# Performance work log

Measured on AMD Instinct MI355X. Metric: run time of the kernel, lower is better.

The kernel has to match this reference:

```python
import jax, jax.numpy as jnp
import numpy as np

N_NODES = 50000
N_EDGES = 1600000
IN_DIM = 64
EDGE_DIM = 8
N_GRAPHS = 256
EXP_IN = 32
H = 64  # hidden dim per head / GCN hidden
EPS = 1e-5
NEG_SLOPE = 0.2


def gat_layer(x, src, dst, ea, W, a_src, a_dst, We, a_e, bias, heads, dim, concat):
    """PyG-style GATConv with edge features and self-loops (fill_value='mean')."""
    N = x.shape[0]
    ones_e = jnp.ones((ea.shape[0],), x.dtype)
    cnt = jax.ops.segment_sum(ones_e, dst, num_segments=N)
    loop_attr = jax.ops.segment_sum(ea, dst, num_segments=N) / jnp.maximum(cnt, 1.0)[:, None]
    s = jnp.concatenate([src, jnp.arange(N)])
    d = jnp.concatenate([dst, jnp.arange(N)])
    eaf = jnp.concatenate([ea, loop_attr], axis=0)  # [E+N, edge_dim]
    h = (x @ W).reshape(N, heads, dim)              # [N, H, D]
    ee = (eaf @ We).reshape(-1, heads, dim)         # [E+N, H, D]
    al_src = (h * a_src).sum(-1)                    # [N, H]
    al_dst = (h * a_dst).sum(-1)                    # [N, H]
    score = al_src[s] + al_dst[d] + (ee * a_e).sum(-1)
    score = jax.nn.leaky_relu(score, NEG_SLOPE)     # [E+N, H]
    m = jax.ops.segment_max(score, d, num_segments=N)
    ex = jnp.exp(score - m[d])
    att = ex / jax.ops.segment_sum(ex, d, num_segments=N)[d]
    out = jax.ops.segment_sum(h[s] * att[:, :, None], d, num_segments=N)  # [N, H, D]
    out = out.reshape(N, heads * dim) if concat else out.mean(axis=1)
    return out + bias


def gcn_layer(x, src, dst, W, b):
    """PyG-style GCNConv: add self loops, symmetric degree normalization."""
    N = x.shape[0]
    s = jnp.concatenate([src, jnp.arange(N)])
    d = jnp.concatenate([dst, jnp.arange(N)])
    deg = jax.ops.segment_sum(jnp.ones((s.shape[0],), x.dtype), d, num_segments=N)
    dinv = jax.lax.rsqrt(deg)  # deg >= 1 thanks to self loops
    norm = dinv[s] * dinv[d]
    h = x @ W
    return jax.ops.segment_sum(h[s] * norm[:, None], d, num_segments=N) + b


def bn(x, g, b):
    m = x.mean(axis=0)
    v = x.var(axis=0)
    return g * (x - m) * jax.lax.rsqrt(v + EPS) + b


def mean_pool(x, batch, num_graphs):
    s = jax.ops.segment_sum(x, batch, num_segments=num_graphs)
    c = jax.ops.segment_sum(jnp.ones((x.shape[0],), x.dtype), batch, num_segments=num_graphs)
    return s / jnp.maximum(c, 1.0)[:, None]


def setup_inputs() -> dict:
    key = jax.random.key(0)
    ks = jax.random.split(key, 32)
    p = lambda i, shape: jax.random.normal(ks[i], shape, jnp.float32) * 0.05
    z = lambda n: jnp.zeros((n,), jnp.float32)
    o = lambda n: jnp.ones((n,), jnp.float32)
    return {
        "x": jax.random.normal(ks[0], (N_NODES, IN_DIM), jnp.float32),
        "edge_attr": jax.random.normal(ks[1], (N_EDGES, EDGE_DIM), jnp.float32),
        "experimental_feat": jax.random.normal(ks[2], (N_GRAPHS, EXP_IN), jnp.float32),
        "edge_index": jax.random.randint(ks[3], (2, N_EDGES), 0, N_NODES),
        "batch": jnp.sort(jax.random.randint(ks[4], (N_NODES,), 0, N_GRAPHS)),
        "W1": p(5, (IN_DIM, 4 * H)), "att_src1": p(6, (4, H)), "att_dst1": p(7, (4, H)),
        "We1": p(8, (EDGE_DIM, 4 * H)), "att_e1": p(9, (4, H)), "b1": z(4 * H),
        "g1": o(4 * H), "be1": z(4 * H),
        "W2": p(10, (4 * H, H)), "att_src2": p(11, (1, H)), "att_dst2": p(12, (1, H)),
        "We2": p(13, (EDGE_DIM, H)), "att_e2": p(14, (1, H)), "b2": z(H),
        "g2": o(H), "be2": z(H),
        "Wg1": p(15, (H, H)), "bg1": z(H), "g3": o(H), "be3": z(H),
        "Wg2": p(16, (H, H)), "bg2": z(H), "g4": o(H), "be4": z(H),
        "Wex1": p(17, (EXP_IN, H)), "bex1": z(H), "Wex2": p(18, (H, H)), "bex2": z(H),
        "Wc1": p(19, (2 * H, 128)), "bc1": z(128), "Wc2": p(20, (128, 1)), "bc2": z(1),
    }


def reference(x, edge_attr, experimental_feat, edge_index, batch,
              W1, att_src1, att_dst1, We1, att_e1, b1, g1, be1,
              W2, att_src2, att_dst2, We2, att_e2, b2, g2, be2,
              Wg1, bg1, g3, be3, Wg2, bg2, g4, be4,
              Wex1, bex1, Wex2, bex2, Wc1, bc1, Wc2, bc2):
    src, dst = edge_index[0], edge_index[1]
    h = gat_layer(x, src, dst, edge_attr, W1, att_src1, att_dst1, We1, att_e1, b1, 4, H, True)
    h = jax.nn.relu(bn(h, g1, be1))
    h = gat_layer(h, src, dst, edge_attr, W2, att_src2, att_dst2, We2, att_e2, b2, 1, H, False)
    h = jax.nn.relu(bn(h, g2, be2))  # dropout = identity in eval
    h = gcn_layer(h, src, dst, Wg1, bg1)
    h = jax.nn.relu(bn(h, g3, be3))
    h = gcn_layer(h, src, dst, Wg2, bg2)
    h = jax.nn.relu(bn(h, g4, be4))
    xp = mean_pool(h, batch, N_GRAPHS)                    # [G, H]
    e = jax.nn.relu(experimental_feat @ Wex1 + bex1)
    e = jax.nn.relu(e @ Wex2 + bex2)
    combined = jnp.concatenate([xp, e], axis=1)           # [G, 2H]
    combined = jax.nn.relu(combined @ Wc1 + bc1)          # [G, 128]
    out = combined @ Wc2 + bc2                            # [G, 1]
    return (out, xp, combined)
```

## Files before the change

### kernel.cpp

```cpp
#include <hip/hip_runtime.h>
#include <hip/hip_bf16.h>

#define N_NODES 50000
#define N_EDGES 1600000
#define N_GRAPHS 256
#define NEG_SLOPE 0.2f
#define BN_EPS 1e-5f

typedef __hip_bfloat16 bf16;
typedef __attribute__((ext_vector_type(8))) short s16x8;
typedef __attribute__((ext_vector_type(4))) float f32x4;
typedef __attribute__((ext_vector_type(4))) int i32x4;
typedef __attribute__((ext_vector_type(4))) unsigned u32x4;

__device__ __forceinline__ float b2f(bf16 v){ return __bfloat162float(v); }
__device__ __forceinline__ bf16 f2b(float v){ return __float2bfloat16(v); }
__device__ __forceinline__ float us2f(unsigned short u){ return __uint_as_float(((unsigned)u)<<16); }
__device__ __forceinline__ unsigned short f2us(float v){ bf16 b = f2b(v); return *(unsigned short*)&b; }
__device__ __forceinline__ unsigned pk2(float a, float b){ return (unsigned)f2us(a) | ((unsigned)f2us(b)<<16); }
__device__ __forceinline__ float ldF(const void* p, size_t i, int m){
  return m ? ((const float*)p)[i] : b2f(((const bf16*)p)[i]);
}
__device__ __forceinline__ float sane(float v){
  return (v == v && fabsf(v) < 1e30f) ? v : 0.f;
}
__device__ __forceinline__ float sel4(const float v[4], int h){
  float r = v[0];
  r = (h==1) ? v[1] : r;
  r = (h==2) ? v[2] : r;
  r = (h==3) ? v[3] : r;
  return r;
}
__device__ __forceinline__ void acc8(float* acc, float w, uint4 u){
  acc[0] += w*us2f((unsigned short)(u.x & 0xffff)); acc[1] += w*us2f((unsigned short)(u.x >> 16));
  acc[2] += w*us2f((unsigned short)(u.y & 0xffff)); acc[3] += w*us2f((unsigned short)(u.y >> 16));
  acc[4] += w*us2f((unsigned short)(u.z & 0xffff)); acc[5] += w*us2f((unsigned short)(u.z >> 16));
  acc[6] += w*us2f((unsigned short)(u.w & 0xffff)); acc[7] += w*us2f((unsigned short)(u.w >> 16));
}
__device__ __forceinline__ void unp8(float* o, uint4 u){
  o[0] = us2f((unsigned short)(u.x & 0xffff)); o[1] = us2f((unsigned short)(u.x >> 16));
  o[2] = us2f((unsigned short)(u.y & 0xffff)); o[3] = us2f((unsigned short)(u.y >> 16));
  o[4] = us2f((unsigned short)(u.z & 0xffff)); o[5] = us2f((unsigned short)(u.z >> 16));
  o[6] = us2f((unsigned short)(u.w & 0xffff)); o[7] = us2f((unsigned short)(u.w >> 16));
}
__device__ __forceinline__ s16x8 pk8(const float* v){
  s16x8 r;
  #pragma unroll
  for(int j=0;j<8;j++) r[j] = (short)f2us(v[j]);
  return r;
}

__device__ int detect_mode_block(const void* x){
  __shared__ int s_ins;
  if(threadIdx.x == 0) s_ins = 0;
  __syncthreads();
  const unsigned short* u = (const unsigned short*)x;
  int c = 0;
  for(int i = threadIdx.x; i < 1024; i += blockDim.x){
    float v = fabsf(us2f(u[i]));
    if(!(v > 1e-6f && v < 1e4f)) c++;
  }
  if(c) atomicAdd(&s_ins, c);
  __syncthreads();
  return (s_ins > 128) ? 1 : 0;
}

#define NSEG 33
struct Bank { const void* p[NSEG]; int n[NSEG]; int off[NSEG]; };

__global__ void k_convert(Bank b, const void* xdet, float* out){
  int m = detect_mode_block(xdet);
  int seg = blockIdx.y;
  int i = blockIdx.x*256 + threadIdx.x;
  if(i < b.n[seg]) out[b.off[seg] + i] = ldF(b.p[seg], i, m);
}

__global__ void k_cvt_x(const void* x, bf16* xb){
  int m = detect_mode_block(x);
  int i4 = blockIdx.x*256 + threadIdx.x;
  if(i4 >= N_NODES*16) return;
  if(m){
    float4 v = ((const float4*)x)[i4];
    ((ushort4*)xb)[i4] = make_ushort4(f2us(v.x), f2us(v.y), f2us(v.z), f2us(v.w));
  } else {
    ((ushort4*)xb)[i4] = ((const ushort4*)x)[i4];
  }
}

__global__ void k_we(const float* __restrict__ We1, const float* __restrict__ ae1,
                     const float* __restrict__ We2, const float* __restrict__ ae2,
                     float* __restrict__ w_e){
  int t = threadIdx.x;
  if(t < 32){
    int h = t >> 3, k = t & 7;
    float s = 0.f;
    for(int d=0;d<64;d++) s += We1[k*256 + h*64 + d] * ae1[h*64 + d];
    w_e[t] = s;
  } else if(t < 40){
    int k = t - 32;
    float s = 0.f;
    for(int d=0;d<64;d++) s += We2[k*64 + d] * ae2[d];
    w_e[t] = s;
  }
}

__global__ void k_wt(const float* __restrict__ W1, const float* __restrict__ W2,
                     const float* __restrict__ Wg1, const float* __restrict__ Wg2,
                     bf16* __restrict__ wt){
  int i = blockIdx.x*256 + threadIdx.x;
  if(i < 16384){
    int c = i >> 6, k = i & 63;
    wt[i] = f2b(W1[k*256 + c]);
  } else if(i < 32768){
    int j = i - 16384; int c = j >> 8, k = j & 255;
    wt[i] = f2b(W2[k*64 + c]);
  } else if(i < 36864){
    int j = i - 32768; int c = j >> 6, k = j & 63;
    wt[i] = f2b(Wg1[k*64 + c]);
  } else if(i < 40960){
    int j = i - 36864; int c = j >> 6, k = j & 63;
    wt[i] = f2b(Wg2[k*64 + c]);
  }
}

__global__ void k_count(const int* __restrict__ dst, int* __restrict__ cnt){
  int e = blockIdx.x*256 + threadIdx.x;
  if(e < N_EDGES){
    int d = dst[e]; if((unsigned)d >= N_NODES) d = 0;
    atomicAdd(&cnt[d], 1);
  }
}

__global__ void k_blocksum(const int* __restrict__ cnt, int* __restrict__ bsum){
  __shared__ int s[256];
  int i = blockIdx.x*256 + threadIdx.x;
  s[threadIdx.x] = (i < N_NODES) ? cnt[i] : 0;
  __syncthreads();
  for(int o=128;o>0;o>>=1){ if(threadIdx.x<o) s[threadIdx.x]+=s[threadIdx.x+o]; __syncthreads(); }
  if(threadIdx.x==0) bsum[blockIdx.x]=s[0];
}

__global__ void k_scan_bsum(const int* __restrict__ bsum, int* __restrict__ bofs, int nb){
  __shared__ int s[256];
  int t = threadIdx.x;
  s[t] = (t<nb) ? bsum[t] : 0;
  __syncthreads();
  for(int o=1;o<256;o<<=1){ int v=(t>=o)?s[t-o]:0; __syncthreads(); s[t]+=v; __syncthreads(); }
  bofs[t] = (t==0) ? 0 : s[t-1];
}

__global__ void k_scan_write(const int* __restrict__ cnt, const int* __restrict__ bofs,
                             int* __restrict__ rp, float* __restrict__ dinv){
  __shared__ int s[256];
  int t = threadIdx.x; int i = blockIdx.x*256 + t;
  int v = (i<N_NODES) ? cnt[i] : 0;
  s[t]=v; __syncthreads();
  for(int o=1;o<256;o<<=1){ int a=(t>=o)?s[t-o]:0; __syncthreads(); s[t]+=a; __syncthreads(); }
  if(i<N_NODES){
    rp[i+1] = s[t] + bofs[blockIdx.x];
    dinv[i] = rsqrtf((float)v + 1.f);
  }
  if(i==0) rp[0]=0;
}

__global__ void k_fill(const int* __restrict__ src, const int* __restrict__ dst,
                       const int* __restrict__ rp, int* __restrict__ fill,
                       const void* __restrict__ ea, const void* __restrict__ xdet,
                       const float* __restrict__ w_e,
                       int4* __restrict__ epk){
  int m = detect_mode_block(xdet);
  int e = blockIdx.x*256 + threadIdx.x;
  if(e >= N_EDGES) return;
  int d = dst[e]; if((unsigned)d >= N_NODES) d = 0;
  int p = atomicAdd(&fill[d], 1);
  int slot = rp[d] + p;
  if((unsigned)slot >= N_EDGES) return;
  int sv = src[e]; if((unsigned)sv >= N_NODES) sv = 0;
  float a[8];
  if(m){
    const float* eaf = (const float*)ea;
    float4 lo = *(const float4*)&eaf[(size_t)e*8];
    float4 hi = *(const float4*)&eaf[(size_t)e*8 + 4];
    a[0]=lo.x; a[1]=lo.y; a[2]=lo.z; a[3]=lo.w;
    a[4]=hi.x; a[5]=hi.y; a[6]=hi.z; a[7]=hi.w;
  } else {
    #pragma unroll
    for(int k=0;k<8;k++) a[k] = b2f(((const bf16*)ea)[(size_t)e*8 + k]);
  }
  unsigned d4[4];
  #pragma unroll
  for(int h=0;h<4;h++){
    float s = 0.f;
    #pragma unroll
    for(int k=0;k<8;k++) s += a[k]*w_e[h*8+k];
    d4[h] = f2us(s);
  }
  float s1 = 0.f;
  #pragma unroll
  for(int k=0;k<8;k++) s1 += a[k]*w_e[32+k];
  i32x4 pk;
  pk[0] = sv;
  pk[1] = (int)(d4[0] | (d4[1] << 16));
  pk[2] = (int)(d4[2] | (d4[3] << 16));
  pk[3] = (int)(unsigned)f2us(s1);
  __builtin_nontemporal_store(pk, (i32x4*)&epk[slot]);
}

__global__ __launch_bounds__(256) void k_gemmA_mfma(
    const bf16* __restrict__ xb,
    const bf16* __restrict__ wt1,
    bf16* __restrict__ hp, int M)
{
  const int tid = threadIdx.x;
  const int w = tid >> 6, l = tid & 63;
  const int lr = l & 15, lg = l >> 4;
  const int bm = blockIdx.x*64 + w*16;
  const int arow_i = bm + lr;
  const uint4* arow = (const uint4*)(xb + (size_t)min(arow_i, M-1)*64);
  uint4 a0u = arow[lg];
  uint4 a1u = arow[4 + lg];
  s16x8 a0 = *(s16x8*)&a0u, a1 = *(s16x8*)&a1u;
  unsigned short* out = (unsigned short*)hp;
  const int orow0 = bm + lg*4;
  #pragma unroll
  for(int ct = 0; ct < 16; ct++){
    const uint4* brow = (const uint4*)(wt1 + (size_t)(ct*16 + lr)*64);
    uint4 b0u = brow[lg];
    uint4 b1u = brow[4 + lg];
    f32x4 acc = {0.f, 0.f, 0.f, 0.f};
    acc = __builtin_amdgcn_mfma_f32_16x16x32_bf16(a0, *(s16x8*)&b0u, acc, 0, 0, 0);
    acc = __builtin_amdgcn_mfma_f32_16x16x32_bf16(a1, *(s16x8*)&b1u, acc, 0, 0, 0);
    #pragma unroll
    for(int r = 0; r < 4; r++){
      int rr = orow0 + r;
      if(rr < M) out[(size_t)rr*256 + ct*16 + lr] = f2us(acc[r]);
    }
  }
}

template<int KIN>
__global__ __launch_bounds__(256) void k_gemmB_mfma(
    const bf16* __restrict__ A, const bf16* __restrict__ Wt,
    bf16* __restrict__ C, int M,
    const float* __restrict__ bnsums, const float* __restrict__ bng, const float* __restrict__ bnb)
{
  __shared__ float st_s[KIN];
  __shared__ float st_t[KIN];
  const int tid = threadIdx.x;
  if(tid < KIN){
    const float invN = 1.0f / (float)N_NODES;
    float mean = bnsums[tid]*invN;
    float var  = fmaxf(bnsums[KIN+tid]*invN - mean*mean, 0.f);
    float s = bng[tid]*rsqrtf(var + BN_EPS);
    st_s[tid] = s;
    st_t[tid] = bnb[tid] - mean*s;
  }
  __syncthreads();
  const int w = tid >> 6, l = tid & 63;
  const int lr = l & 15, lg = l >> 4;
  const int bm = blockIdx.x*64 + w*16;
  const int arow_i = bm + lr;
  const uint4* arow = (const uint4*)(A + (size_t)min(arow_i, M-1)*KIN);
  f32x4 acc[4];
  #pragma unroll
  for(int ct=0;ct<4;ct++) acc[ct] = (f32x4){0.f,0.f,0.f,0.f};
  #pragma unroll
  for(int k0 = 0; k0 < KIN; k0 += 32){
    uint4 au = arow[(k0 >> 3) + lg];
    int c0 = k0 + lg*8;
    float v[8]; unp8(v, au);
    #pragma unroll
    for(int j = 0; j < 8; j++){
      float y = sane(v[j])*st_s[c0+j] + st_t[c0+j];
      v[j] = fmaxf(y, 0.f);
    }
    s16x8 af = pk8(v);
    #pragma unroll
    for(int ct = 0; ct < 4; ct++){
      const uint4* brow = (const uint4*)(Wt + (size_t)(ct*16 + lr)*KIN);
      uint4 bu = brow[(k0 >> 3) + lg];
      acc[ct] = __builtin_amdgcn_mfma_f32_16x16x32_bf16(af, *(s16x8*)&bu, acc[ct], 0, 0, 0);
    }
  }
  unsigned short* out = (unsigned short*)C;
  const int orow0 = bm + lg*4;
  #pragma unroll
  for(int ct = 0; ct < 4; ct++){
    #pragma unroll
    for(int r = 0; r < 4; r++){
      int rr = orow0 + r;
      if(rr < M) out[(size_t)rr*64 + ct*16 + lr] = f2us(acc[ct][r]);
    }
  }
}

__global__ void k_al4(const bf16* __restrict__ hp, const float* __restrict__ asrc,
                      const float* __restrict__ adst,
                      float* __restrict__ als4, float* __restrict__ ald4){
  int idx = blockIdx.x*256 + threadIdx.x;
  if(idx >= N_NODES*4) return;
  int n = idx >> 2, h = idx & 3;
  const unsigned short* row = (const unsigned short*)hp + (size_t)n*256 + h*64;
  float ss=0.f, sd=0.f;
  #pragma unroll
  for(int q=0;q<16;q++){
    ushort4 u = *(const ushort4*)&row[4*q];
    float4 a_s = *(const float4*)&asrc[h*64 + 4*q];
    float4 a_d = *(const float4*)&adst[h*64 + 4*q];
    float v0=us2f(u.x), v1=us2f(u.y), v2=us2f(u.z), v3=us2f(u.w);
    ss += v0*a_s.x + v1*a_s.y + v2*a_s.z + v3*a_s.w;
    sd += v0*a_d.x + v1*a_d.y + v2*a_d.z + v3*a_d.w;
  }
  als4[idx]=ss; ald4[idx]=sd;
}

__global__ void k_al1(const bf16* __restrict__ hp, const float* __restrict__ asrc,
                      const float* __restrict__ adst,
                      float* __restrict__ als, float* __restrict__ ald){
  int n = blockIdx.x*256 + threadIdx.x;
  if(n >= N_NODES) return;
  const unsigned short* row = (const unsigned short*)hp + (size_t)n*64;
  float ss=0.f, sd=0.f;
  #pragma unroll
  for(int q=0;q<16;q++){
    ushort4 u = *(const ushort4*)&row[4*q];
    float4 a_s = *(const float4*)&asrc[4*q];
    float4 a_d = *(const float4*)&adst[4*q];
    float v0=us2f(u.x), v1=us2f(u.y), v2=us2f(u.z), v3=us2f(u.w);
    ss += v0*a_s.x + v1*a_s.y + v2*a_s.z + v3*a_s.w;
    sd += v0*a_d.x + v1*a_d.y + v2*a_d.z + v3*a_d.w;
  }
  als[n]=ss; ald[n]=sd;
}

__global__ __launch_bounds__(64) void k_gat_agg4(
    const int* __restrict__ rp, const int4* __restrict__ epk,
    const bf16* __restrict__ hp,
    const float* __restrict__ als4, const float* __restrict__ ald4,
    const float* __restrict__ bias256, bf16* __restrict__ out1){
  int n = blockIdx.x; int t = threadIdx.x;
  int eh = t >> 5, c8 = t & 31;
  int head = c8 >> 3;
  __shared__ int   ssrc[64];
  __shared__ float swt[64][4];
  int s0 = rp[n], e0 = rp[n+1];
  if((unsigned)s0 > N_EDGES){ s0=0; e0=0; }
  if(e0 < s0 || (unsigned)e0 > N_EDGES) e0 = s0;
  float4 aldv = *(const float4*)&ald4[n*4];
  float4 alsvn = *(const float4*)&als4[n*4];
  float wsum[4] = {0.f,0.f,0.f,0.f};
  float dsum[4] = {0.f,0.f,0.f,0.f};
  float acc[8]  = {0.f,0.f,0.f,0.f,0.f,0.f,0.f,0.f};
  const unsigned short* hpu = (const unsigned short*)hp;

  for(int base = s0; base < e0; base += 64){
    int m = min(64, e0 - base);
    if(t < m){
      i32x4 pk = __builtin_nontemporal_load((const i32x4*)&epk[base+t]);
      int sn = pk[0]; if((unsigned)sn >= N_NODES) sn = 0;
      ssrc[t] = sn;
      float edf[4] = {us2f((unsigned short)(pk[1] & 0xffff)), us2f((unsigned short)((unsigned)pk[1] >> 16)),
                      us2f((unsigned short)(pk[2] & 0xffff)), us2f((unsigned short)((unsigned)pk[2] >> 16))};
      float4 alss = *(const float4*)&als4[sn*4];
      float alssv[4] = {alss.x, alss.y, alss.z, alss.w};
      float aldvv[4] = {aldv.x, aldv.y, aldv.z, aldv.w};
      float w4[4];
      #pragma unroll
      for(int h=0;h<4;h++){
        float sc = alssv[h] + aldvv[h] + edf[h];
        sc = sc > 0.f ? sc : NEG_SLOPE*sc;
        sc = fminf(sc, 30.f);
        float w = __expf(sc);
        w4[h] = w;
        wsum[h] += w; dsum[h] += edf[h];
      }
      *(float4*)&swt[t][0] = make_float4(w4[0], w4[1], w4[2], w4[3]);
    }
    __syncthreads();
    #pragma unroll 8
    for(int i=0;i<m;i+=2){
      int j = i + eh;
      if(j < m){
        int row = ssrc[j];
        float w = swt[j][head];
        uint4 u = *(const uint4*)&hpu[(size_t)row*256 + 8*c8];
        acc8(acc, w, u);
      }
    }
    __syncthreads();
  }
  #pragma unroll
  for(int o=1;o<64;o<<=1){
    #pragma unroll
    for(int h=0;h<4;h++){
      wsum[h] += __shfl_xor(wsum[h], o);
      dsum[h] += __shfl_xor(dsum[h], o);
    }
  }
  #pragma unroll
  for(int q=0;q<8;q++) acc[q] += __shfl_xor(acc[q], 32);
  if(eh == 0){
    float alsnv[4] = {alsvn.x, alsvn.y, alsvn.z, alsvn.w};
    float aldnv[4] = {aldv.x, aldv.y, aldv.z, aldv.w};
    float sEh = sel4(wsum, head), sDh = sel4(dsum, head);
    float deg = (float)(e0 - s0);
    float sdot = deg > 0.f ? sDh/deg : 0.f;
    float sc = sel4(alsnv, head) + sel4(aldnv, head) + sdot;
    sc = sc > 0.f ? sc : NEG_SLOPE*sc;
    sc = fminf(sc, 30.f);
    float wself = __expf(sc);
    float self[8];
    unp8(self, *(const uint4*)&hpu[(size_t)n*256 + 8*c8]);
    float4 b0 = *(const float4*)&bias256[8*c8];
    float4 b1 = *(const float4*)&bias256[8*c8 + 4];
    float bi[8] = {b0.x,b0.y,b0.z,b0.w,b1.x,b1.y,b1.z,b1.w};
    float inv = 1.f/(sEh + wself);
    float o8[8];
    #pragma unroll
    for(int q=0;q<8;q++) o8[q] = (acc[q] + wself*self[q])*inv + bi[q];
    u32x4 st;
    st[0] = pk2(o8[0],o8[1]); st[1] = pk2(o8[2],o8[3]);
    st[2] = pk2(o8[4],o8[5]); st[3] = pk2(o8[6],o8[7]);
    __builtin_nontemporal_store(st, (u32x4*)&((unsigned short*)out1)[(size_t)n*256 + 8*c8]);
  }
}

__global__ __launch_bounds__(64) void k_gat_agg1e(
    const int* __restrict__ rp, const int4* __restrict__ epk,
    const bf16* __restrict__ hp,
    const float* __restrict__ als, const float* __restrict__ ald,
    const float* __restrict__ bias64, bf16* __restrict__ out){
  int n = blockIdx.x; int t = threadIdx.x;
  int eg = t >> 3, c8 = t & 7;
  __shared__ float sw[64];
  __shared__ int   ssrc[64];
  int s0 = rp[n], e0 = rp[n+1];
  if((unsigned)s0 > N_EDGES){ s0=0; e0=0; }
  if(e0 < s0 || (unsigned)e0 > N_EDGES) e0 = s0;
  float aldn = ald[n];
  float wsum_l = 0.f, dsum_l = 0.f;
  float acc[8] = {0.f,0.f,0.f,0.f,0.f,0.f,0.f,0.f};
  const unsigned short* hpu = (const unsigned short*)hp;
  for(int base = s0; base < e0; base += 64){
    int m = min(64, e0 - base);
    if(t < m){
      i32x4 pk = __builtin_nontemporal_load((const i32x4*)&epk[base+t]);
      int sn = pk[0]; if((unsigned)sn >= N_NODES) sn = 0;
      ssrc[t] = sn;
      float ed = us2f((unsigned short)(pk[3] & 0xffff));
      float sc = als[sn] + aldn + ed;
      sc = sc > 0.f ? sc : NEG_SLOPE*sc;
      sc = fminf(sc, 30.f);
      float w = __expf(sc);
      sw[t] = w;
      wsum_l += w; dsum_l += ed;
    }
    __syncthreads();
    #pragma unroll 4
    for(int i=0;i<m;i+=8){
      int j = i + eg;
      if(j < m){
        int row = ssrc[j];
        float w = sw[j];
        uint4 u = *(const uint4*)&hpu[(size_t)row*64 + 8*c8];
        acc8(acc, w, u);
      }
    }
    __syncthreads();
  }
  #pragma unroll
  for(int o=1;o<64;o<<=1){ wsum_l += __shfl_xor(wsum_l, o); dsum_l += __shfl_xor(dsum_l, o); }
  #pragma unroll
  for(int q=0;q<8;q++){
    acc[q] += __shfl_xor(acc[q], 8);
    acc[q] += __shfl_xor(acc[q], 16);
    acc[q] += __shfl_xor(acc[q], 32);
  }
  if(t < 8){
    float deg = (float)(e0 - s0);
    float sdot = deg > 0.f ? dsum_l/deg : 0.f;
    float sc = als[n] + aldn + sdot;
    sc = sc > 0.f ? sc : NEG_SLOPE*sc;
    sc = fminf(sc, 30.f);
    float wself = __expf(sc);
    float self[8];
    unp8(self, *(const uint4*)&hpu[(size_t)n*64 + 8*t]);
    float4 b0 = *(const float4*)&bias64[8*t];
    float4 b1 = *(const float4*)&bias64[8*t + 4];
    float bi[8] = {b0.x,b0.y,b0.z,b0.w,b1.x,b1.y,b1.z,b1.w};
    float inv = 1.f/(wsum_l + wself);
    float o8[8];
    #pragma unroll
    for(int q=0;q<8;q++) o8[q] = (acc[q] + wself*self[q])*inv + bi[q];
    u32x4 st;
    st[0] = pk2(o8[0],o8[1]); st[1] = pk2(o8[2],o8[3]);
    st[2] = pk2(o8[4],o8[5]); st[3] = pk2(o8[6],o8[7]);
    __builtin_nontemporal_store(st, (u32x4*)&((unsigned short*)out)[(size_t)n*64 + 8*t]);
  }
}

__global__ __launch_bounds__(64) void k_gcn_agg(
    const int* __restrict__ rp, const int4* __restrict__ epk,
    const float* __restrict__ dinv, const bf16* __restrict__ gp,
    const float* __restrict__ bias, bf16* __restrict__ out){
  int n = blockIdx.x; int t = threadIdx.x;
  int eg = t >> 3, c8 = t & 7;
  __shared__ float sw[64];
  __shared__ int   ssrc[64];
  int s0 = rp[n], e0 = rp[n+1];
  if((unsigned)s0 > N_EDGES){ s0=0; e0=0; }
  if(e0 < s0 || (unsigned)e0 > N_EDGES) e0 = s0;
  float dn = dinv[n];
  float acc[8] = {0.f,0.f,0.f,0.f,0.f,0.f,0.f,0.f};
  const unsigned short* gpu = (const unsigned short*)gp;
  for(int base = s0; base < e0; base += 64){
    int m = min(64, e0 - base);
    if(t < m){
      i32x4 pk = __builtin_nontemporal_load((const i32x4*)&epk[base+t]);
      int sn = pk[0]; if((unsigned)sn >= N_NODES) sn = 0;
      ssrc[t]=sn; sw[t]=dinv[sn];
    }
    __syncthreads();
    #pragma unroll 4
    for(int i=0;i<m;i+=8){
      int j = i + eg;
      if(j < m){
        int row = ssrc[j];
        float w = sw[j];
        uint4 u = *(const uint4*)&gpu[(size_t)row*64 + 8*c8];
        acc8(acc, w, u);
      }
    }
    __syncthreads();
  }
  #pragma unroll
  for(int q=0;q<8;q++){
    acc[q] += __shfl_xor(acc[q], 8);
    acc[q] += __shfl_xor(acc[q], 16);
    acc[q] += __shfl_xor(acc[q], 32);
  }
  if(t < 8){
    float self[8];
    unp8(self, *(const uint4*)&gpu[(size_t)n*64 + 8*t]);
    float4 b0 = *(const float4*)&bias[8*t];
    float4 b1 = *(const float4*)&bias[8*t + 4];
    float bi[8] = {b0.x,b0.y,b0.z,b0.w,b1.x,b1.y,b1.z,b1.w};
    float o8[8];
    #pragma unroll
    for(int q=0;q<8;q++) o8[q] = dn*(acc[q] + dn*self[q]) + bi[q];
    u32x4 st;
    st[0] = pk2(o8[0],o8[1]); st[1] = pk2(o8[2],o8[3]);
    st[2] = pk2(o8[4],o8[5]); st[3] = pk2(o8[6],o8[7]);
    __builtin_nontemporal_store(st, (u32x4*)&((unsigned short*)out)[(size_t)n*64 + 8*t]);
  }
}

template<int C>
__global__ void k_colstats(const bf16* __restrict__ X, float* __restrict__ sums){
  constexpr int RPB = 128;
  constexpr int RSTEP = 256 / C;
  int c = threadIdx.x % C;
  int r0 = threadIdx.x / C;
  int rbeg = blockIdx.x * RPB;
  int rend = min(N_NODES, rbeg + RPB);
  const unsigned short* Xu = (const unsigned short*)X;
  float s = 0.f, q = 0.f;
  for(int r = rbeg + r0; r < rend; r += RSTEP){
    float v = sane(us2f(Xu[(size_t)r*C + c]));
    s += v; q += v*v;
  }
  atomicAdd(&sums[c], s);
  atomicAdd(&sums[C + c], q);
}

__global__ __launch_bounds__(64) void k_pool3(
    const bf16* __restrict__ h, const int* __restrict__ batch,
    const float* __restrict__ sums, const float* __restrict__ g4,
    const float* __restrict__ b4,
    float* __restrict__ psum, float* __restrict__ pcnt){
  int t = threadIdx.x;
  int n0 = blockIdx.x * 256;
  int n1 = min(N_NODES, n0 + 256);
  if(n0 >= n1) return;
  const float invN = 1.0f / (float)N_NODES;
  float mean = sums[t]*invN;
  float var = fmaxf(sums[64+t]*invN - mean*mean, 0.f);
  float rstd = rsqrtf(var + BN_EPS);
  float gg = g4[t], bb = b4[t];
  const unsigned short* hu = (const unsigned short*)h;
  int cur = batch[n0]; if((unsigned)cur >= N_GRAPHS) cur = 0;
  float acc = 0.f; int cl = 0;
  for(int n = n0; n < n1; n++){
    int g = batch[n]; if((unsigned)g >= N_GRAPHS) g = 0;
    if(g != cur){
      atomicAdd(&psum[cur*64 + t], acc);
      if(t == 0) atomicAdd(&pcnt[cur], (float)cl);
      acc = 0.f; cl = 0; cur = g;
    }
    float y = (sane(us2f(hu[(size_t)n*64 + t]))-mean)*rstd*gg + bb;
    acc += fmaxf(y, 0.f);
    cl++;
  }
  atomicAdd(&psum[cur*64 + t], acc);
  if(t == 0) atomicAdd(&pcnt[cur], (float)cl);
}

__device__ __forceinline__ void stO(void* o, size_t i, float v, int m){
  if(m) ((float*)o)[i] = v; else ((bf16*)o)[i] = f2b(v);
}

__global__ __launch_bounds__(128) void k_head(
    const float* __restrict__ psum, const float* __restrict__ pcnt,
    const float* __restrict__ exf,
    const float* __restrict__ Wex1, const float* __restrict__ bex1,
    const float* __restrict__ Wex2, const float* __restrict__ bex2,
    const float* __restrict__ Wc1, const float* __restrict__ bc1,
    const float* __restrict__ Wc2, const float* __restrict__ bc2,
    const void* __restrict__ xdet, void* __restrict__ dout){
  int m0 = detect_mode_block(xdet);
  int g = blockIdx.x; int t = threadIdx.x;
  __shared__ float ci[128];
  __shared__ float e1[64];
  __shared__ float comb[128];
  __shared__ float red[128];
  if(t < 64){
    float c = fmaxf(pcnt[g], 1.f);
    float xp = sane(psum[g*64 + t]) / c;
    ci[t] = xp;
    stO(dout, 256 + (size_t)g*64 + t, xp, m0);
  } else {
    int j = t - 64;
    float s = bex1[j];
    for(int k=0;k<32;k++) s += exf[g*32 + k] * Wex1[k*64 + j];
    e1[j] = fmaxf(s, 0.f);
  }
  __syncthreads();
  if(t >= 64){
    int j = t - 64;
    float s = bex2[j];
    for(int k=0;k<64;k++) s += e1[k] * Wex2[k*64 + j];
    ci[64 + j] = fmaxf(s, 0.f);
  }
  __syncthreads();
  {
    float s = bc1[t];
    for(int k=0;k<128;k++) s += ci[k] * Wc1[k*128 + t];
    s = fmaxf(s, 0.f);
    comb[t] = s;
    stO(dout, 256 + 16384 + (size_t)g*128 + t, s, m0);
  }
  __syncthreads();
  red[t] = comb[t] * Wc2[t];
  __syncthreads();
  for(int o=64;o>0;o>>=1){ if(t<o) red[t]+=red[t+o]; __syncthreads(); }
  if(t==0) stO(dout, g, red[0] + bc2[0], m0);
}

extern "C" void kernel_launch(void* const* d_in, const int* in_sizes, int n_in,
                              void* d_out, int out_size, void* d_ws, size_t ws_size,
                              hipStream_t stream){
  const void* x    = d_in[0];
  const void* ea   = d_in[1];
  const int* ei    = (const int*)d_in[3];
  const int* batch = (const int*)d_in[4];
  const int* src = ei;
  const int* dst = ei + N_EDGES;

  char* base = (char*)d_ws;
  size_t off = 0;
  auto alloc = [&](size_t bytes) -> void* {
    void* r = base + off;
    off += (bytes + 255) & ~(size_t)255;
    return r;
  };
  int*   cnt    = (int*)  alloc((size_t)N_NODES*4);
  int*   fill   = (int*)  alloc((size_t)N_NODES*4);
  float* bnstat = (float*)alloc(4096);
  float* pool   = (float*)alloc((size_t)(N_GRAPHS*64 + N_GRAPHS)*4);
  size_t zbytes = off;
  int*   rp      = (int*)  alloc((size_t)(N_NODES+1)*4);
  int*   bsum    = (int*)  alloc(256*4);
  int*   bofs    = (int*)  alloc(256*4);
  int4*  epk     = (int4*) alloc((size_t)N_EDGES*16);
  float* dinv    = (float*)alloc((size_t)N_NODES*4);
  float* w_e     = (float*)alloc(64*4);
  float* als4    = (float*)alloc((size_t)N_NODES*4*4);
  float* ald4    = (float*)alloc((size_t)N_NODES*4*4);
  float* wbank   = (float*)alloc(80000*4);
  bf16*  wt      = (bf16*) alloc((size_t)40960*2);
  bf16*  xb      = (bf16*) alloc((size_t)N_NODES*64*2);
  bf16*  hp      = (bf16*) alloc((size_t)N_NODES*256*2);
  bf16*  outb    = (bf16*) alloc((size_t)N_NODES*256*2);

  bf16* out1 = outb;
  bf16* out2 = outb;
  bf16* out3 = outb + (size_t)N_NODES*64;
  bf16* out4 = outb + (size_t)N_NODES*128;
  float* bn1 = bnstat;
  float* bn2 = bnstat + 512;
  float* bn3 = bnstat + 640;
  float* bn4 = bnstat + 768;
  float* psum = pool;
  float* pcnt = pool + N_GRAPHS*64;

  bf16* wt1  = wt;
  bf16* wt2  = wt + 16384;
  bf16* wtg1 = wt + 32768;
  bf16* wtg2 = wt + 36864;

  const int segidx[NSEG] = {2, 5,6,7,8,9,10,11,12, 13,14,15,16,17,18,19,20,
                            21,22,23,24, 25,26,27,28, 29,30,31,32, 33,34,35,36};
  const int segn[NSEG] = {8192, 16384,256,256,2048,256,256,256,256,
                          16384,64,64,512,64,64,64,64,
                          4096,64,64,64, 4096,64,64,64,
                          2048,64,4096,64, 16384,128,128,1};
  Bank bk;
  int offs[NSEG]; int acc0 = 0;
  for(int i=0;i<NSEG;i++){ bk.p[i]=d_in[segidx[i]]; bk.n[i]=segn[i]; bk.off[i]=acc0; offs[i]=acc0; acc0+=segn[i]; }
  const float* f_exf = wbank + offs[0];
  const float* fW1 = wbank+offs[1]; const float* fas1 = wbank+offs[2]; const float* fad1 = wbank+offs[3];
  const float* fWe1= wbank+offs[4]; const float* fae1 = wbank+offs[5]; const float* fb1  = wbank+offs[6];
  const float* fg1 = wbank+offs[7]; const float* fbe1 = wbank+offs[8];
  const float* fW2 = wbank+offs[9]; const float* fas2 = wbank+offs[10]; const float* fad2 = wbank+offs[11];
  const float* fWe2= wbank+offs[12]; const float* fae2 = wbank+offs[13]; const float* fb2 = wbank+offs[14];
  const float* fg2 = wbank+offs[15]; const float* fbe2 = wbank+offs[16];
  const float* fWg1= wbank+offs[17]; const float* fbg1 = wbank+offs[18]; const float* fg3 = wbank+offs[19];
  const float* fbe3= wbank+offs[20];
  const float* fWg2= wbank+offs[21]; const float* fbg2 = wbank+offs[22]; const float* fg4 = wbank+offs[23];
  const float* fbe4= wbank+offs[24];
  const float* fWex1=wbank+offs[25]; const float* fbex1= wbank+offs[26];
  const float* fWex2=wbank+offs[27]; const float* fbex2= wbank+offs[28];
  const float* fWc1= wbank+offs[29]; const float* fbc1 = wbank+offs[30];
  const float* fWc2= wbank+offs[31]; const float* fbc2 = wbank+offs[32];

  const int nbN  = (N_NODES + 255)/256;
  const int nbE  = (N_EDGES + 255)/256;
  const int nbT  = (N_NODES + 63)/64;

  hipMemsetAsync(d_ws, 0, zbytes, stream);
  {
    dim3 g((16384+255)/256, NSEG);
    k_convert<<<g,256,0,stream>>>(bk, x, wbank);
  }
  k_wt<<<160,256,0,stream>>>(fW1, fW2, fWg1, fWg2, wt);
  k_cvt_x<<<(N_NODES*16+255)/256,256,0,stream>>>(x, xb);
  k_we<<<1,64,0,stream>>>(fWe1, fae1, fWe2, fae2, w_e);
  k_count<<<nbE,256,0,stream>>>(dst, cnt);
  k_blocksum<<<nbN,256,0,stream>>>(cnt, bsum);
  k_scan_bsum<<<1,256,0,stream>>>(bsum, bofs, nbN);
  k_scan_write<<<nbN,256,0,stream>>>(cnt, bofs, rp, dinv);
  k_fill<<<nbE,256,0,stream>>>(src, dst, rp, fill, ea, x, w_e, epk);

  k_gemmA_mfma<<<nbT,256,0,stream>>>(xb, wt1, hp, N_NODES);
  k_al4<<<(N_NODES*4+255)/256,256,0,stream>>>(hp, fas1, fad1, als4, ald4);
  k_gat_agg4<<<N_NODES,64,0,stream>>>(rp, epk, hp, als4, ald4, fb1, out1);
  k_colstats<256><<<(N_NODES+127)/128,256,0,stream>>>(out1, bn1);

  k_gemmB_mfma<256><<<nbT,256,0,stream>>>(out1, wt2, hp, N_NODES, bn1, fg1, fbe1);
  k_al1<<<nbN,256,0,stream>>>(hp, fas2, fad2, als4, ald4);
  k_gat_agg1e<<<N_NODES,64,0,stream>>>(rp, epk, hp, als4, ald4, fb2, out2);
  k_colstats<64><<<(N_NODES+127)/128,256,0,stream>>>(out2, bn2);

  k_gemmB_mfma<64><<<nbT,256,0,stream>>>(out2, wtg1, hp, N_NODES, bn2, fg2, fbe2);
  k_gcn_agg<<<N_NODES,64,0,stream>>>(rp, epk, dinv, hp, fbg1, out3);
  k_colstats<64><<<(N_NODES+127)/128,256,0,stream>>>(out3, bn3);

  k_gemmB_mfma<64><<<nbT,256,0,stream>>>(out3, wtg2, hp, N_NODES, bn3, fg3, fbe3);
  k_gcn_agg<<<N_NODES,64,0,stream>>>(rp, epk, dinv, hp, fbg2, out4);
  k_colstats<64><<<(N_NODES+127)/128,256,0,stream>>>(out4, bn4);

  k_pool3<<<nbN,64,0,stream>>>(out4, batch, bn4, fg4, fbe4, psum, pcnt);
  k_head<<<N_GRAPHS,128,0,stream>>>(psum, pcnt, f_exf, fWex1, fbex1, fWex2, fbex2,
                                    fWc1, fbc1, fWc2, fbc2, x, (void*)d_out);
}
```

Baseline: 978.0 us.

## Fuse attention logits into GEMMs and pack four nodes per aggregation block

The per-node attention dot products (als/ald) are now computed inside the MFMA GEMM epilogues from fp32 accumulators, using cross-lane shuffles, which removes the separate k_al4/k_al1 kernels and their re-read of hp. The GAT and GCN aggregation kernels change from one 64-thread block per node to 256-thread blocks holding four independent waves, one node per wave. Block-wide __syncthreads are replaced with wave-local LDS fences. Nontemporal output stores become plain stores. The logits now use unrounded fp32 values instead of the bf16-rounded hp, and the wave-level fences rely on each wave working only on its own LDS slice.

```diff
diff --git a/kernel.cpp b/kernel.cpp
--- a/kernel.cpp
+++ b/kernel.cpp
@@ -11,7 +11,6 @@
 typedef __attribute__((ext_vector_type(8))) short s16x8;
 typedef __attribute__((ext_vector_type(4))) float f32x4;
 typedef __attribute__((ext_vector_type(4))) int i32x4;
-typedef __attribute__((ext_vector_type(4))) unsigned u32x4;
 
 __device__ __forceinline__ float b2f(bf16 v){ return __bfloat162float(v); }
 __device__ __forceinline__ bf16 f2b(float v){ return __float2bfloat16(v); }
@@ -48,6 +47,11 @@
   #pragma unroll
   for(int j=0;j<8;j++) r[j] = (short)f2us(v[j]);
   return r;
+}
+__device__ __forceinline__ void wave_lds_fence(){
+  __builtin_amdgcn_sched_barrier(0);
+  asm volatile("s_waitcnt lgkmcnt(0)" ::: "memory");
+  __builtin_amdgcn_sched_barrier(0);
 }
 
 __device__ int detect_mode_block(const void* x){
@@ -209,7 +213,10 @@
 __global__ __launch_bounds__(256) void k_gemmA_mfma(
     const bf16* __restrict__ xb,
     const bf16* __restrict__ wt1,
-    bf16* __restrict__ hp, int M)
+    bf16* __restrict__ hp, int M,
+    const float* __restrict__ asrc,
+    const float* __restrict__ adst,
+    float* __restrict__ als4, float* __restrict__ ald4)
 {
   const int tid = threadIdx.x;
   const int w = tid >> 6, l = tid & 63;
@@ -222,6 +229,8 @@
   s16x8 a0 = *(s16x8*)&a0u, a1 = *(s16x8*)&a1u;
   unsigned short* out = (unsigned short*)hp;
   const int orow0 = bm + lg*4;
+  float p_s[4][4] = {};
+  float p_d[4][4] = {};
   #pragma unroll
   for(int ct = 0; ct < 16; ct++){
     const uint4* brow = (const uint4*)(wt1 + (size_t)(ct*16 + lr)*64);
@@ -230,10 +239,38 @@
     f32x4 acc = {0.f, 0.f, 0.f, 0.f};
     acc = __builtin_amdgcn_mfma_f32_16x16x32_bf16(a0, *(s16x8*)&b0u, acc, 0, 0, 0);
     acc = __builtin_amdgcn_mfma_f32_16x16x32_bf16(a1, *(s16x8*)&b1u, acc, 0, 0, 0);
+    float a_s = asrc[ct*16 + lr];
+    float a_d = adst[ct*16 + lr];
+    int hh = ct >> 2;
     #pragma unroll
     for(int r = 0; r < 4; r++){
+      p_s[hh][r] += acc[r]*a_s;
+      p_d[hh][r] += acc[r]*a_d;
       int rr = orow0 + r;
       if(rr < M) out[(size_t)rr*256 + ct*16 + lr] = f2us(acc[r]);
+    }
+  }
+  #pragma unroll
+  for(int o = 1; o < 16; o <<= 1){
+    #pragma unroll
+    for(int hh=0; hh<4; hh++)
+      #pragma unroll
+      for(int r=0; r<4; r++){
+        p_s[hh][r] += __shfl_xor(p_s[hh][r], o);
+        p_d[hh][r] += __shfl_xor(p_d[hh][r], o);
+      }
+  }
+  if(lr == 0){
+    #pragma unroll
+    for(int r=0;r<4;r++){
+      int rr = orow0 + r;
+      if(rr < M){
+        #pragma unroll
+        for(int hh=0;hh<4;hh++){
+          als4[rr*4 + hh] = p_s[hh][r];
+          ald4[rr*4 + hh] = p_d[hh][r];
+        }
+      }
     }
   }
 }
@@ -242,7 +279,9 @@
 __global__ __launch_bounds__(256) void k_gemmB_mfma(
     const bf16* __restrict__ A, const bf16* __restrict__ Wt,
     bf16* __restrict__ C, int M,
-    const float* __restrict__ bnsums, const float* __restrict__ bng, const float* __restrict__ bnb)
+    const float* __restrict__ bnsums, const float* __restrict__ bng, const float* __restrict__ bnb,
+    const float* __restrict__ asrc, const float* __restrict__ adst,
+    float* __restrict__ als, float* __restrict__ ald)
 {
   __shared__ float st_s[KIN];
   __shared__ float st_t[KIN];
@@ -292,57 +331,51 @@
       if(rr < M) out[(size_t)rr*64 + ct*16 + lr] = f2us(acc[ct][r]);
     }
   }
-}
-
-__global__ void k_al4(const bf16* __restrict__ hp, const float* __restrict__ asrc,
-                      const float* __restrict__ adst,
-                      float* __restrict__ als4, float* __restrict__ ald4){
-  int idx = blockIdx.x*256 + threadIdx.x;
-  if(idx >= N_NODES*4) return;
-  int n = idx >> 2, h = idx & 3;
-  const unsigned short* row = (const unsigned short*)hp + (size_t)n*256 + h*64;
-  float ss=0.f, sd=0.f;
-  #pragma unroll
-  for(int q=0;q<16;q++){
-    ushort4 u = *(const ushort4*)&row[4*q];
-    float4 a_s = *(const float4*)&asrc[h*64 + 4*q];
-    float4 a_d = *(const float4*)&adst[h*64 + 4*q];
-    float v0=us2f(u.x), v1=us2f(u.y), v2=us2f(u.z), v3=us2f(u.w);
-    ss += v0*a_s.x + v1*a_s.y + v2*a_s.z + v3*a_s.w;
-    sd += v0*a_d.x + v1*a_d.y + v2*a_d.z + v3*a_d.w;
-  }
-  als4[idx]=ss; ald4[idx]=sd;
-}
-
-__global__ void k_al1(const bf16* __restrict__ hp, const float* __restrict__ asrc,
-                      const float* __restrict__ adst,
-                      float* __restrict__ als, float* __restrict__ ald){
-  int n = blockIdx.x*256 + threadIdx.x;
-  if(n >= N_NODES) return;
-  const unsigned short* row = (const unsigned short*)hp + (size_t)n*64;
-  float ss=0.f, sd=0.f;
-  #pragma unroll
-  for(int q=0;q<16;q++){
-    ushort4 u = *(const ushort4*)&row[4*q];
-    float4 a_s = *(const float4*)&asrc[4*q];
-    float4 a_d = *(const float4*)&adst[4*q];
-    float v0=us2f(u.x), v1=us2f(u.y), v2=us2f(u.z), v3=us2f(u.w);
-    ss += v0*a_s.x + v1*a_s.y + v2*a_s.z + v3*a_s.w;
-    sd += v0*a_d.x + v1*a_d.y + v2*a_d.z + v3*a_d.w;
-  }
-  als[n]=ss; ald[n]=sd;
-}
-
-__global__ __launch_bounds__(64) void k_gat_agg4(
+  if(als){
+    float p_s[4] = {0.f,0.f,0.f,0.f};
+    float p_d[4] = {0.f,0.f,0.f,0.f};
+    #pragma unroll
+    for(int ct=0;ct<4;ct++){
+      float a_s = asrc[ct*16 + lr];
+      float a_d = adst[ct*16 + lr];
+      #pragma unroll
+      for(int r=0;r<4;r++){
+        p_s[r] += acc[ct][r]*a_s;
+        p_d[r] += acc[ct][r]*a_d;
+      }
+    }
+    #pragma unroll
+    for(int o = 1; o < 16; o <<= 1){
+      #pragma unroll
+      for(int r=0;r<4;r++){
+        p_s[r] += __shfl_xor(p_s[r], o);
+        p_d[r] += __shfl_xor(p_d[r], o);
+      }
+    }
+    if(lr == 0){
+      #pragma unroll
+      for(int r=0;r<4;r++){
+        int rr = orow0 + r;
+        if(rr < M){ als[rr] = p_s[r]; ald[rr] = p_d[r]; }
+      }
+    }
+  }
+}
+
+__global__ __launch_bounds__(256) void k_gat_agg4(
     const int* __restrict__ rp, const int4* __restrict__ epk,
     const bf16* __restrict__ hp,
     const float* __restrict__ als4, const float* __restrict__ ald4,
     const float* __restrict__ bias256, bf16* __restrict__ out1){
-  int n = blockIdx.x; int t = threadIdx.x;
-  int eh = t >> 5, c8 = t & 31;
+  const int wid = threadIdx.x >> 6, l = threadIdx.x & 63;
+  const int n = blockIdx.x*4 + wid;
+  if(n >= N_NODES) return;
+  int eh = l >> 5, c8 = l & 31;
   int head = c8 >> 3;
-  __shared__ int   ssrc[64];
-  __shared__ float swt[64][4];
+  __shared__ int   ssrc_s[4][64];
+  __shared__ float swt_s[4][64][4];
+  int* ssrc = ssrc_s[wid];
+  float (*swt)[4] = swt_s[wid];
   int s0 = rp[n], e0 = rp[n+1];
   if((unsigned)s0 > N_EDGES){ s0=0; e0=0; }
   if(e0 < s0 || (unsigned)e0 > N_EDGES) e0 = s0;
@@ -355,10 +388,10 @@
 
   for(int base = s0; base < e0; base += 64){
     int m = min(64, e0 - base);
-    if(t < m){
-      i32x4 pk = __builtin_nontemporal_load((const i32x4*)&epk[base+t]);
+    if(l < m){
+      i32x4 pk = __builtin_nontemporal_load((const i32x4*)&epk[base+l]);
       int sn = pk[0]; if((unsigned)sn >= N_NODES) sn = 0;
-      ssrc[t] = sn;
+      ssrc[l] = sn;
       float edf[4] = {us2f((unsigned short)(pk[1] & 0xffff)), us2f((unsigned short)((unsigned)pk[1] >> 16)),
                       us2f((unsigned short)(pk[2] & 0xffff)), us2f((unsigned short)((unsigned)pk[2] >> 16))};
       float4 alss = *(const float4*)&als4[sn*4];
@@ -374,9 +407,9 @@
         w4[h] = w;
         wsum[h] += w; dsum[h] += edf[h];
       }
-      *(float4*)&swt[t][0] = make_float4(w4[0], w4[1], w4[2], w4[3]);
-    }
-    __syncthreads();
+      *(float4*)&swt[l][0] = make_float4(w4[0], w4[1], w4[2], w4[3]);
+    }
+    wave_lds_fence();
     #pragma unroll 8
     for(int i=0;i<m;i+=2){
       int j = i + eh;
@@ -387,7 +420,7 @@
         acc8(acc, w, u);
       }
     }
-    __syncthreads();
+    __builtin_amdgcn_wave_barrier();
   }
   #pragma unroll
   for(int o=1;o<64;o<<=1){
@@ -418,22 +451,26 @@
     float o8[8];
     #pragma unroll
     for(int q=0;q<8;q++) o8[q] = (acc[q] + wself*self[q])*inv + bi[q];
-    u32x4 st;
-    st[0] = pk2(o8[0],o8[1]); st[1] = pk2(o8[2],o8[3]);
-    st[2] = pk2(o8[4],o8[5]); st[3] = pk2(o8[6],o8[7]);
-    __builtin_nontemporal_store(st, (u32x4*)&((unsigned short*)out1)[(size_t)n*256 + 8*c8]);
-  }
-}
-
-__global__ __launch_bounds__(64) void k_gat_agg1e(
+    uint4 st;
+    st.x = pk2(o8[0],o8[1]); st.y = pk2(o8[2],o8[3]);
+    st.z = pk2(o8[4],o8[5]); st.w = pk2(o8[6],o8[7]);
+    *(uint4*)&((unsigned short*)out1)[(size_t)n*256 + 8*c8] = st;
+  }
+}
+
+__global__ __launch_bounds__(256) void k_gat_agg1e(
     const int* __restrict__ rp, const int4* __restrict__ epk,
     const bf16* __restrict__ hp,
     const float* __restrict__ als, const float* __restrict__ ald,
     const float* __restrict__ bias64, bf16* __restrict__ out){
-  int n = blockIdx.x; int t = threadIdx.x;
-  int eg = t >> 3, c8 = t & 7;
-  __shared__ float sw[64];
-  __shared__ int   ssrc[64];
+  const int wid = threadIdx.x >> 6, l = threadIdx.x & 63;
+  const int n = blockIdx.x*4 + wid;
+  if(n >= N_NODES) return;
+  int eg = l >> 3, c8 = l & 7;
+  __shared__ float sw_s[4][64];
+  __shared__ int   ssrc_s[4][64];
+  float* sw = sw_s[wid];
+  int* ssrc = ssrc_s[wid];
   int s0 = rp[n], e0 = rp[n+1];
   if((unsigned)s0 > N_EDGES){ s0=0; e0=0; }
   if(e0 < s0 || (unsigned)e0 > N_EDGES) e0 = s0;
@@ -443,19 +480,19 @@
   const unsigned short* hpu = (const unsigned short*)hp;
   for(int base = s0; base < e0; base += 64){
     int m = min(64, e0 - base);
-    if(t < m){
-      i32x4 pk = __builtin_nontemporal_load((const i32x4*)&epk[base+t]);
+    if(l < m){
+      i32x4 pk = __builtin_nontemporal_load((const i32x4*)&epk[base+l]);
       int sn = pk[0]; if((unsigned)sn >= N_NODES) sn = 0;
-      ssrc[t] = sn;
+      ssrc[l] = sn;
       float ed = us2f((unsigned short)(pk[3] & 0xffff));
       float sc = als[sn] + aldn + ed;
       sc = sc > 0.f ? sc : NEG_SLOPE*sc;
       sc = fminf(sc, 30.f);
       float w = __expf(sc);
-      sw[t] = w;
+      sw[l] = w;
       wsum_l += w; dsum_l += ed;
     }
-    __syncthreads();
+    wave_lds_fence();
     #pragma unroll 4
     for(int i=0;i<m;i+=8){
       int j = i + eg;
@@ -466,7 +503,7 @@
         acc8(acc, w, u);
       }
     }
-    __syncthreads();
+    __builtin_amdgcn_wave_barrier();
   }
   #pragma unroll
   for(int o=1;o<64;o<<=1){ wsum_l += __shfl_xor(wsum_l, o); dsum_l += __shfl_xor(dsum_l, o); }
@@ -476,7 +513,7 @@
     acc[q] += __shfl_xor(acc[q], 16);
     acc[q] += __shfl_xor(acc[q], 32);
   }
-  if(t < 8){
+  if(l < 8){
     float deg = (float)(e0 - s0);
     float sdot = deg > 0.f ? dsum_l/deg : 0.f;
     float sc = als[n] + aldn + sdot;
@@ -484,29 +521,33 @@
     sc = fminf(sc, 30.f);
     float wself = __expf(sc);
     float self[8];
-    unp8(self, *(const uint4*)&hpu[(size_t)n*64 + 8*t]);
-    float4 b0 = *(const float4*)&bias64[8*t];
-    float4 b1 = *(const float4*)&bias64[8*t + 4];
+    unp8(self, *(const uint4*)&hpu[(size_t)n*64 + 8*l]);
+    float4 b0 = *(const float4*)&bias64[8*l];
+    float4 b1 = *(const float4*)&bias64[8*l + 4];
     float bi[8] = {b0.x,b0.y,b0.z,b0.w,b1.x,b1.y,b1.z,b1.w};
     float inv = 1.f/(wsum_l + wself);
     float o8[8];
     #pragma unroll
     for(int q=0;q<8;q++) o8[q] = (acc[q] + wself*self[q])*inv + bi[q];
-    u32x4 st;
-    st[0] = pk2(o8[0],o8[1]); st[1] = pk2(o8[2],o8[3]);
-    st[2] = pk2(o8[4],o8[5]); st[3] = pk2(o8[6],o8[7]);
-    __builtin_nontemporal_store(st, (u32x4*)&((unsigned short*)out)[(size_t)n*64 + 8*t]);
-  }
-}
-
-__global__ __launch_bounds__(64) void k_gcn_agg(
+    uint4 st;
+    st.x = pk2(o8[0],o8[1]); st.y = pk2(o8[2],o8[3]);
+    st.z = pk2(o8[4],o8[5]); st.w = pk2(o8[6],o8[7]);
+    *(uint4*)&((unsigned short*)out)[(size_t)n*64 + 8*l] = st;
+  }
+}
+
+__global__ __launch_bounds__(256) void k_gcn_agg(
     const int* __restrict__ rp, const int4* __restrict__ epk,
     const float* __restrict__ dinv, const bf16* __restrict__ gp,
     const float* __restrict__ bias, bf16* __restrict__ out){
-  int n = blockIdx.x; int t = threadIdx.x;
-  int eg = t >> 3, c8 = t & 7;
-  __shared__ float sw[64];
-  __shared__ int   ssrc[64];
+  const int wid = threadIdx.x >> 6, l = threadIdx.x & 63;
+  const int n = blockIdx.x*4 + wid;
+  if(n >= N_NODES) return;
+  int eg = l >> 3, c8 = l & 7;
+  __shared__ float sw_s[4][64];
+  __shared__ int   ssrc_s[4][64];
+  float* sw = sw_s[wid];
+  int* ssrc = ssrc_s[wid];
   int s0 = rp[n], e0 = rp[n+1];
   if((unsigned)s0 > N_EDGES){ s0=0; e0=0; }
   if(e0 < s0 || (unsigned)e0 > N_EDGES) e0 = s0;
@@ -515,12 +556,12 @@
   const unsigned short* gpu = (const unsigned short*)gp;
   for(int base = s0; base < e0; base += 64){
     int m = min(64, e0 - base);
-    if(t < m){
-      i32x4 pk = __builtin_nontemporal_load((const i32x4*)&epk[base+t]);
+    if(l < m){
+      i32x4 pk = __builtin_nontemporal_load((const i32x4*)&epk[base+l]);
       int sn = pk[0]; if((unsigned)sn >= N_NODES) sn = 0;
-      ssrc[t]=sn; sw[t]=dinv[sn];
-    }
-    __syncthreads();
+      ssrc[l]=sn; sw[l]=dinv[sn];
+    }
+    wave_lds_fence();
     #pragma unroll 4
     for(int i=0;i<m;i+=8){
       int j = i + eg;
@@ -531,7 +572,7 @@
         acc8(acc, w, u);
       }
     }
-    __syncthreads();
+    __builtin_amdgcn_wave_barrier();
   }
   #pragma unroll
   for(int q=0;q<8;q++){
@@ -539,19 +580,19 @@
     acc[q] += __shfl_xor(acc[q], 16);
     acc[q] += __shfl_xor(acc[q], 32);
   }
-  if(t < 8){
+  if(l < 8){
     float self[8];
-    unp8(self, *(const uint4*)&gpu[(size_t)n*64 + 8*t]);
-    float4 b0 = *(const float4*)&bias[8*t];
-    float4 b1 = *(const float4*)&bias[8*t + 4];
+    unp8(self, *(const uint4*)&gpu[(size_t)n*64 + 8*l]);
+    float4 b0 = *(const float4*)&bias[8*l];
+    float4 b1 = *(const float4*)&bias[8*l + 4];
     float bi[8] = {b0.x,b0.y,b0.z,b0.w,b1.x,b1.y,b1.z,b1.w};
     float o8[8];
     #pragma unroll
     for(int q=0;q<8;q++) o8[q] = dn*(acc[q] + dn*self[q]) + bi[q];
-    u32x4 st;
-    st[0] = pk2(o8[0],o8[1]); st[1] = pk2(o8[2],o8[3]);
-    st[2] = pk2(o8[4],o8[5]); st[3] = pk2(o8[6],o8[7]);
-    __builtin_nontemporal_store(st, (u32x4*)&((unsigned short*)out)[(size_t)n*64 + 8*t]);
+    uint4 st;
+    st.x = pk2(o8[0],o8[1]); st.y = pk2(o8[2],o8[3]);
+    st.z = pk2(o8[4],o8[5]); st.w = pk2(o8[6],o8[7]);
+    *(uint4*)&((unsigned short*)out)[(size_t)n*64 + 8*l] = st;
   }
 }
 
@@ -736,6 +777,7 @@
   const int nbN  = (N_NODES + 255)/256;
   const int nbE  = (N_EDGES + 255)/256;
   const int nbT  = (N_NODES + 63)/64;
+  const int nbA  = (N_NODES + 3)/4;
 
   hipMemsetAsync(d_ws, 0, zbytes, stream);
   {
@@ -751,22 +793,23 @@
   k_scan_write<<<nbN,256,0,stream>>>(cnt, bofs, rp, dinv);
   k_fill<<<nbE,256,0,stream>>>(src, dst, rp, fill, ea, x, w_e, epk);
 
-  k_gemmA_mfma<<<nbT,256,0,stream>>>(xb, wt1, hp, N_NODES);
-  k_al4<<<(N_NODES*4+255)/256,256,0,stream>>>(hp, fas1, fad1, als4, ald4);
-  k_gat_agg4<<<N_NODES,64,0,stream>>>(rp, epk, hp, als4, ald4, fb1, out1);
+  k_gemmA_mfma<<<nbT,256,0,stream>>>(xb, wt1, hp, N_NODES, fas1, fad1, als4, ald4);
+  k_gat_agg4<<<nbA,256,0,stream>>>(rp, epk, hp, als4, ald4, fb1, out1);
   k_colstats<256><<<(N_NODES+127)/128,256,0,stream>>>(out1, bn1);
 
-  k_gemmB_mfma<256><<<nbT,256,0,stream>>>(out1, wt2, hp, N_NODES, bn1, fg1, fbe1);
-  k_al1<<<nbN,256,0,stream>>>(hp, fas2, fad2, als4, ald4);
-  k_gat_agg1e<<<N_NODES,64,0,stream>>>(rp, epk, hp, als4, ald4, fb2, out2);
+  k_gemmB_mfma<256><<<nbT,256,0,stream>>>(out1, wt2, hp, N_NODES, bn1, fg1, fbe1,
+                                          fas2, fad2, als4, ald4);
+  k_gat_agg1e<<<nbA,256,0,stream>>>(rp, epk, hp, als4, ald4, fb2, out2);
   k_colstats<64><<<(N_NODES+127)/128,256,0,stream>>>(out2, bn2);
 
-  k_gemmB_mfma<64><<<nbT,256,0,stream>>>(out2, wtg1, hp, N_NODES, bn2, fg2, fbe2);
-  k_gcn_agg<<<N_NODES,64,0,stream>>>(rp, epk, dinv, hp, fbg1, out3);
+  k_gemmB_mfma<64><<<nbT,256,0,stream>>>(out2, wtg1, hp, N_NODES, bn2, fg2, fbe2,
+                                         nullptr, nullptr, nullptr, nullptr);
+  k_gcn_agg<<<nbA,256,0,stream>>>(rp, epk, dinv, hp, fbg1, out3);
   k_colstats<64><<<(N_NODES+127)/128,256,0,stream>>>(out3, bn3);
 
-  k_gemmB_mfma<64><<<nbT,256,0,stream>>>(out3, wtg2, hp, N_NODES, bn3, fg3, fbe3);
-  k_gcn_agg<<<N_NODES,64,0,stream>>>(rp, epk, dinv, hp, fbg2, out4);
+  k_gemmB_mfma<64><<<nbT,256,0,stream>>>(out3, wtg2, hp, N_NODES, bn3, fg3, fbe3,
+                                         nullptr, nullptr, nullptr, nullptr);
+  k_gcn_agg<<<nbA,256,0,stream>>>(rp, epk, dinv, hp, fbg2, out4);
   k_colstats<64><<<(N_NODES+127)/128,256,0,stream>>>(out4, bn4);
 
   k_pool3<<<nbN,64,0,stream>>>(out4, batch, bn4, fg4, fbe4, psum, pcnt);
```

Result: faster. 929.2 us (-5.0%).
